# Performance work log

Measured on AMD Instinct MI355X. Metric: run time of the kernel, lower is better.

## Reference

```python
import jax, jax.numpy as jnp
import numpy as np

EMBED_DIM = 1024
HEAD_NUM = 16
HEAD_DIM = EMBED_DIM // HEAD_NUM
T, B, S = 2048, 4, 2048


def setup_inputs() -> dict:
    key = jax.random.key(0)
    ks = jax.random.split(key, 11)
    s = 0.02
    return {
        "query": jax.random.normal(ks[0], (T, B, EMBED_DIM), jnp.float32),
        "key": jax.random.normal(ks[1], (S, B, EMBED_DIM), jnp.float32),
        "value": jax.random.normal(ks[2], (S, B, EMBED_DIM), jnp.float32),
        "q_proj_weight": jax.random.normal(ks[3], (EMBED_DIM, EMBED_DIM), jnp.float32) * s,
        "k_proj_weight": jax.random.normal(ks[4], (EMBED_DIM, EMBED_DIM), jnp.float32) * s,
        "v_proj_weight": jax.random.normal(ks[5], (EMBED_DIM, EMBED_DIM), jnp.float32) * s,
        "in_proj_bias": jax.random.normal(ks[6], (3 * EMBED_DIM,), jnp.float32) * s,
        "bias_k": jax.random.normal(ks[7], (1, 1, EMBED_DIM), jnp.float32) * s,
        "bias_v": jax.random.normal(ks[8], (1, 1, EMBED_DIM), jnp.float32) * s,
        "out_proj_weight": jax.random.normal(ks[9], (EMBED_DIM, EMBED_DIM), jnp.float32) * s,
        "out_proj_bias": jax.random.normal(ks[10], (EMBED_DIM,), jnp.float32) * s,
    }


def reference(query, key, value, q_proj_weight, k_proj_weight, v_proj_weight,
              in_proj_bias, bias_k, bias_v, out_proj_weight, out_proj_bias):
    t, b, e = query.shape
    h, hd = HEAD_NUM, HEAD_DIM
    scaling = float(hd) ** -0.5
    # input projections (F.linear: x @ W.T + b)
    q = (query @ q_proj_weight.T + in_proj_bias[:e]) * scaling          # [T,B,E]
    k = key @ k_proj_weight.T + in_proj_bias[e:2 * e]                   # [S,B,E]
    v = value @ v_proj_weight.T + in_proj_bias[2 * e:]                  # [S,B,E]
    # append bias_k / bias_v token along the sequence dim
    k = jnp.concatenate([k, jnp.broadcast_to(bias_k, (1, b, e))], axis=0)  # [S+1,B,E]
    v = jnp.concatenate([v, jnp.broadcast_to(bias_v, (1, b, e))], axis=0)  # [S+1,B,E]
    # split heads: [L, B, E] -> [B*H, L, hd]
    q = q.reshape(t, b * h, hd).transpose(1, 0, 2)
    k = k.reshape(-1, b * h, hd).transpose(1, 0, 2)
    v = v.reshape(-1, b * h, hd).transpose(1, 0, 2)
    # full O(T*S) attention, as in the original bmm->softmax->bmm
    weights = jax.nn.softmax(jnp.einsum('nqd,nkd->nqk', q, k), axis=-1)  # [B*H,T,S+1]
    out = jnp.einsum('nqk,nkd->nqd', weights, v)                         # [B*H,T,hd]
    out = out.transpose(1, 0, 2).reshape(t, b, e)
    out = out @ out_proj_weight.T + out_proj_bias
    avg_weights = weights.sum(axis=1) / h                                # [B*H,S+1]
    return out, avg_weights
```

## Files before the change

kernel.cpp:

```cpp
#include <hip/hip_runtime.h>

#define T_DIM 2048
#define B_DIM 4
#define S_DIM 2048
#define E_DIM 1024
#define H_NUM 16
#define HD    64
#define NH    64
#define SP1   2049
#define SPAD  2112
#define NCHUNK 33
#define NTOKE ((size_t)T_DIM * B_DIM * E_DIM)

typedef short bf16x8 __attribute__((ext_vector_type(8)));
typedef short bf16x4 __attribute__((ext_vector_type(4)));
typedef float f32x4  __attribute__((ext_vector_type(4)));
typedef float f32x16 __attribute__((ext_vector_type(16)));
typedef unsigned int u32;

#define QSCALE 0.18033688011112042f

#if __has_builtin(__builtin_amdgcn_exp2f)
__device__ __forceinline__ float exp2_fast(float x) { return __builtin_amdgcn_exp2f(x); }
#else
__device__ __forceinline__ float exp2_fast(float x) { return __expf(x * 0.6931471805599453f); }
#endif

__device__ __forceinline__ unsigned short f2bf(float x) {
    union { float f; unsigned int u; } v; v.f = x;
    unsigned int r = v.u + 0x7FFFu + ((v.u >> 16) & 1u);
    return (unsigned short)(r >> 16);
}

__device__ __forceinline__ u32 cvtpk_bf16(float lo, float hi) {
    u32 r;
    asm("v_cvt_pk_bf16_f32 %0, %1, %2" : "=v"(r) : "v"(lo), "v"(hi));
    return r;
}
__device__ __forceinline__ void plswap(u32& a, u32& b) {
    asm("v_permlane32_swap_b32 %0, %1" : "+v"(a), "+v"(b));
}
__device__ __forceinline__ float max3f(float a, float b, float c) {
    float d;
    asm("v_max3_f32 %0, %1, %2, %3" : "=v"(d) : "v"(a), "v"(b), "v"(c));
    return d;
}

__device__ __forceinline__ void load_lds16(const void* g, void* l) {
    __builtin_amdgcn_global_load_lds(
        (const __attribute__((address_space(1))) unsigned int*)g,
        (__attribute__((address_space(3))) unsigned int*)l, 16, 0, 0);
}

__global__ __launch_bounds__(256)
void cvt_all(const float* __restrict__ q, const float* __restrict__ k,
             const float* __restrict__ v, const float* __restrict__ w0,
             const float* __restrict__ w1, const float* __restrict__ w2,
             const float* __restrict__ w3, short* __restrict__ indst,
             short* __restrict__ wdst, short* __restrict__ k_h,
             short* __restrict__ v_h, const float* __restrict__ bias_k,
             const float* __restrict__ bias_v)
{
    const int y = blockIdx.y;
    if (y < 3) {
        const float* src = (y == 0) ? q : (y == 1) ? k : v;
        short* d = indst + (size_t)y * NTOKE;
        const size_t i = (size_t)blockIdx.x * 256 + threadIdx.x;
        const float4* s = reinterpret_cast<const float4*>(src) + i * 2;
        float4 a = s[0], b = s[1];
        uint4 o;
        o.x = cvtpk_bf16(a.x, a.y); o.y = cvtpk_bf16(a.z, a.w);
        o.z = cvtpk_bf16(b.x, b.y); o.w = cvtpk_bf16(b.z, b.w);
        *(reinterpret_cast<uint4*>(d) + i) = o;
    } else {
        const size_t gi = (size_t)blockIdx.x * 256 + threadIdx.x;
        const size_t per = (size_t)E_DIM * E_DIM / 8;
        if (gi < 4 * per) {
            const int wsel = (int)(gi / per);
            const size_t i = gi % per;
            const float* src = (wsel == 0) ? w0 : (wsel == 1) ? w1 : (wsel == 2) ? w2 : w3;
            short* d = wdst + (size_t)wsel * E_DIM * E_DIM;
            const float4* s = reinterpret_cast<const float4*>(src) + i * 2;
            float4 a = s[0], b = s[1];
            uint4 o;
            o.x = cvtpk_bf16(a.x, a.y); o.y = cvtpk_bf16(a.z, a.w);
            o.z = cvtpk_bf16(b.x, b.y); o.w = cvtpk_bf16(b.z, b.w);
            *(reinterpret_cast<uint4*>(d) + i) = o;
        } else {
            const size_t fi = gi - 4 * per;
            if (fi < (size_t)(SPAD - S_DIM) * NH * HD) {
                const int d   = (int)(fi & 63);
                const int row = (int)((fi >> 6) & 63);
                const int n   = (int)(fi >> 12);
                short bk = 0, bv = 0;
                if (row == 0) {
                    bk = (short)f2bf(bias_k[(n & 15) * HD + d]);
                    bv = (short)f2bf(bias_v[(n & 15) * HD + d]);
                }
                const size_t idx = ((size_t)n * SPAD + S_DIM + row) * HD + d;
                k_h[idx] = bk;
                v_h[idx] = bv;
            }
        }
    }
}

__global__ __launch_bounds__(256, 4)
void gemm_qkv(const short* __restrict__ Abase, const short* __restrict__ Wall,
              const float* __restrict__ biasAll, short* __restrict__ outp)
{
    __shared__ short As[2][128][32];
    __shared__ short Bs[2][128][32];
    const int bm = blockIdx.x, bn = blockIdx.y;
    const int z = blockIdx.z;
    const short* Az = Abase + (size_t)z * NTOKE;
    const short* W  = Wall + (size_t)z * E_DIM * E_DIM;
    const float* bias = biasAll + z * E_DIM;

    const int tid = threadIdx.x;
    const int l = tid & 63, w = tid >> 6;
    const int wr = w >> 1, wc = w & 1;
    const int lr = l & 15, lg = l >> 4;
    const int srow = tid >> 2, scol = (tid & 3) * 8;

    auto stage = [&](int b, int k0) {
#pragma unroll
        for (int r = 0; r < 2; ++r) {
            const int row = r * 64 + srow;
            load_lds16(Az + (size_t)(bm * 128 + row) * E_DIM + k0 + scol, &As[b][row][scol]);
            load_lds16(W + (size_t)(bn * 128 + row) * E_DIM + k0 + scol, &Bs[b][row][scol]);
        }
    };

    stage(0, 0);
    __syncthreads();

    f32x4 acc[4][4] = {};
    int buf = 0;

    for (int k0 = 0; k0 < E_DIM; k0 += 32) {
        if (k0 + 32 < E_DIM) stage(buf ^ 1, k0 + 32);

        __builtin_amdgcn_s_setprio(1);
        bf16x8 af[4], bf[4];
#pragma unroll
        for (int mi = 0; mi < 4; ++mi)
            af[mi] = *reinterpret_cast<const bf16x8*>(&As[buf][wr * 64 + mi * 16 + lr][lg * 8]);
#pragma unroll
        for (int ni = 0; ni < 4; ++ni)
            bf[ni] = *reinterpret_cast<const bf16x8*>(&Bs[buf][wc * 64 + ni * 16 + lr][lg * 8]);
#pragma unroll
        for (int mi = 0; mi < 4; ++mi)
#pragma unroll
            for (int ni = 0; ni < 4; ++ni)
                acc[mi][ni] = __builtin_amdgcn_mfma_f32_16x16x32_bf16(
                    af[mi], bf[ni], acc[mi][ni], 0, 0, 0);
        __builtin_amdgcn_s_setprio(0);
        __syncthreads();
        buf ^= 1;
    }

#pragma unroll
    for (int mi = 0; mi < 4; ++mi)
#pragma unroll
        for (int ni = 0; ni < 4; ++ni) {
            const int colg = bn * 128 + wc * 64 + ni * 16 + lr;
            const float bv = bias[colg];
#pragma unroll
            for (int r = 0; r < 4; ++r) {
                const int m = bm * 128 + wr * 64 + mi * 16 + lg * 4 + r;
                float v = acc[mi][ni][r] + bv;
                if (z == 0) v *= QSCALE;
                const int seq = m >> 2, b = m & 3;
                const int head = colg >> 6, d = colg & 63;
                const int sd = (z == 0) ? T_DIM : SPAD;
                short* ob = outp;
                if (z == 1) ob += (size_t)NH * T_DIM * HD;
                else if (z == 2) ob += (size_t)NH * T_DIM * HD + (size_t)NH * SPAD * HD;
                ob[((size_t)(b * 16 + head) * sd + seq) * HD + d] = (short)f2bf(v);
            }
        }
}

__global__ __launch_bounds__(256, 2)
void gemm_out(const short* __restrict__ o_h, const short* __restrict__ wob,
              const float* __restrict__ out_b, float* __restrict__ out)
{
    __shared__ short As[2][128][64];
    __shared__ short Bs[2][128][64];
    const int bm = blockIdx.x, bn = blockIdx.y;

    const int tid = threadIdx.x;
    const int l = tid & 63, w = tid >> 6;
    const int wr = w >> 1, wc = w & 1;
    const int lr = l & 15, lg = l >> 4;
    const int srow = tid >> 3, scol = (tid & 7) * 8;

    auto stage = [&](int b, int k0) {
#pragma unroll
        for (int r = 0; r < 4; ++r) {
            const int row = r * 32 + srow;
            const int m = bm * 128 + row;
            const short* ga = o_h +
                ((size_t)((m & 3) * 16 + (k0 >> 6)) * T_DIM + (m >> 2)) * HD + scol;
            load_lds16(ga, &As[b][row][scol]);
            load_lds16(wob + (size_t)(bn * 128 + row) * E_DIM + k0 + scol, &Bs[b][row][scol]);
        }
    };

    stage(0, 0);
    __syncthreads();

    f32x4 acc[4][4] = {};
    int buf = 0;

    for (int k0 = 0; k0 < E_DIM; k0 += 64) {
        if (k0 + 64 < E_DIM) stage(buf ^ 1, k0 + 64);

        __builtin_amdgcn_s_setprio(1);
#pragma unroll
        for (int c = 0; c < 2; ++c) {
            bf16x8 af[4], bf[4];
#pragma unroll
            for (int mi = 0; mi < 4; ++mi)
                af[mi] = *reinterpret_cast<const bf16x8*>(&As[buf][wr * 64 + mi * 16 + lr][c * 32 + lg * 8]);
#pragma unroll
            for (int ni = 0; ni < 4; ++ni)
                bf[ni] = *reinterpret_cast<const bf16x8*>(&Bs[buf][wc * 64 + ni * 16 + lr][c * 32 + lg * 8]);
#pragma unroll
            for (int mi = 0; mi < 4; ++mi)
#pragma unroll
                for (int ni = 0; ni < 4; ++ni)
                    acc[mi][ni] = __builtin_amdgcn_mfma_f32_16x16x32_bf16(
                        af[mi], bf[ni], acc[mi][ni], 0, 0, 0);
        }
        __builtin_amdgcn_s_setprio(0);
        __syncthreads();
        buf ^= 1;
    }

#pragma unroll
    for (int mi = 0; mi < 4; ++mi)
#pragma unroll
        for (int ni = 0; ni < 4; ++ni) {
            const int colg = bn * 128 + wc * 64 + ni * 16 + lr;
            const float bv = out_b[colg];
#pragma unroll
            for (int r = 0; r < 4; ++r) {
                const int m = bm * 128 + wr * 64 + mi * 16 + lg * 4 + r;
                out[(size_t)m * E_DIM + colg] = acc[mi][ni][r] + bv;
            }
        }
}

__global__ __launch_bounds__(512, 4)
void attn_mfma(const short* __restrict__ q_h, const short* __restrict__ k_h,
               const short* __restrict__ v_h, short* __restrict__ o_h,
               float* __restrict__ m_arr, float* __restrict__ l_arr)
{
    __shared__ short KsD[2][64 * 64];
    __shared__ short VtD[2][64 * 64];

    const int id = blockIdx.x;
    const int xcd = id & 7, slot = id >> 3;
    const int n = xcd * 8 + (slot >> 3);
    const int q0 = (slot & 7) * 256;

    const int tid = threadIdx.x, l = tid & 63, w = tid >> 6;
    const int ql = l & 31;
    const int hi = l >> 5;
    const int qrow = q0 + w * 32 + ql;

    const int krow = tid >> 3, kcg = tid & 7;
    const int kswz = (kcg * 16) ^ ((krow & 7) << 4);
    const int sp = tid & 31, dq = tid >> 5;

    const short* kbase = k_h + (size_t)n * SPAD * HD;
    const short* vbase = v_h + (size_t)n * SPAD * HD;

    bf16x8 aq0, aq1, aq2, aq3;
    {
        const short* qp = q_h + ((size_t)n * T_DIM + qrow) * HD + hi * 8;
        aq0 = *(const bf16x8*)(qp);
        aq1 = *(const bf16x8*)(qp + 16);
        aq2 = *(const bf16x8*)(qp + 32);
        aq3 = *(const bf16x8*)(qp + 48);
    }

    bf16x8 pk  = *(const bf16x8*)(kbase + (size_t)krow * HD + kcg * 8);
    bf16x4 pva = *(const bf16x4*)(vbase + (size_t)(2 * sp) * HD + dq * 4);
    bf16x4 pvb = *(const bf16x4*)(vbase + (size_t)(2 * sp + 1) * HD + dq * 4);
    {
        char* KsB = (char*)KsD[0];
        char* VtB = (char*)VtD[0];
        *(bf16x8*)(KsB + krow * 128 + kswz) = pk;
#pragma unroll
        for (int j = 0; j < 4; ++j) {
            u32 pkd = (u32)(unsigned short)pva[j] | ((u32)(unsigned short)pvb[j] << 16);
            const int d = dq * 4 + j;
            *(u32*)(VtB + d * 128 + ((4 * sp) ^ ((d & 7) << 4))) = pkd;
        }
    }
    __syncthreads();

    float m_run = 0.0f;
    float l_run = 0.0f;
    f32x16 accA, accB;
#pragma unroll
    for (int r = 0; r < 16; ++r) { accA[r] = 0.f; accB[r] = 0.f; }

    for (int kc = 0; kc < NCHUNK; ++kc) {
        const char* KsB = (const char*)KsD[kc & 1];
        const char* VtB = (const char*)VtD[kc & 1];
        const bool more = (kc + 1 < NCHUNK);

        if (more) {
            const int s0n = (kc + 1) * 64;
            pk  = *(const bf16x8*)(kbase + (size_t)(s0n + krow) * HD + kcg * 8);
            pva = *(const bf16x4*)(vbase + (size_t)(s0n + 2 * sp) * HD + dq * 4);
            pvb = *(const bf16x4*)(vbase + (size_t)(s0n + 2 * sp + 1) * HD + dq * 4);
        }

        f32x16 sc0, sc1;
        const float nm = -m_run;
#pragma unroll
        for (int r = 0; r < 16; ++r) { sc0[r] = nm; sc1[r] = nm; }
        __builtin_amdgcn_s_setprio(1);
#pragma unroll
        for (int sl = 0; sl < 4; ++sl) {
            const int cb = ((sl * 32) + hi * 16) ^ ((ql & 7) << 4);
            bf16x8 kf0 = *(const bf16x8*)(KsB + ql * 128 + cb);
            bf16x8 kf1 = *(const bf16x8*)(KsB + (32 + ql) * 128 + cb);
            bf16x8 qf = (sl == 0) ? aq0 : (sl == 1) ? aq1 : (sl == 2) ? aq2 : aq3;
            sc0 = __builtin_amdgcn_mfma_f32_32x32x16_bf16(kf0, qf, sc0, 0, 0, 0);
            sc1 = __builtin_amdgcn_mfma_f32_32x32x16_bf16(kf1, qf, sc1, 0, 0, 0);
        }
        __builtin_amdgcn_s_setprio(0);

        const int s0 = kc * 64;
        if (s0 + 64 > SP1) {
#pragma unroll
            for (int r = 0; r < 16; ++r) {
                const int key = (r & 3) + 8 * (r >> 2) + 4 * hi;
                if (s0 + key >= SP1)      sc0[r] = -1e30f;
                if (s0 + 32 + key >= SP1) sc1[r] = -1e30f;
            }
        }

        float a0 = max3f(sc0[0],  sc0[1],  sc0[2]);
        float a1 = max3f(sc0[3],  sc0[4],  sc0[5]);
        float a2 = max3f(sc0[6],  sc0[7],  sc0[8]);
        float a3 = max3f(sc0[9],  sc0[10], sc0[11]);
        float a4 = max3f(sc0[12], sc0[13], sc0[14]);
        float a5 = max3f(sc0[15], sc1[0],  sc1[1]);
        float a6 = max3f(sc1[2],  sc1[3],  sc1[4]);
        float a7 = max3f(sc1[5],  sc1[6],  sc1[7]);
        float a8 = max3f(sc1[8],  sc1[9],  sc1[10]);
        float a9 = max3f(sc1[11], sc1[12], sc1[13]);
        float aA = fmaxf(sc1[14], sc1[15]);
        float b0 = max3f(a0, a1, a2);
        float b1 = max3f(a3, a4, a5);
        float b2 = max3f(a6, a7, a8);
        float b3 = fmaxf(a9, aA);
        float mxl = fmaxf(max3f(b0, b1, b2), b3);
        const float mx = fmaxf(mxl, __shfl_xor(mxl, 32));
        if (!__all(mx <= 8.0f)) {
            const float sh = fmaxf(mx, 0.0f);
            const float fac = exp2_fast(-sh);
            l_run *= fac;
#pragma unroll
            for (int r = 0; r < 16; ++r) {
                accA[r] *= fac; accB[r] *= fac;
                sc0[r] -= sh;   sc1[r] -= sh;
            }
            m_run += sh;
        }
        float p0[16], p1[16];
#pragma unroll
        for (int r = 0; r < 16; ++r) p0[r] = exp2_fast(sc0[r]);
#pragma unroll
        for (int r = 0; r < 16; ++r) p1[r] = exp2_fast(sc1[r]);
        float sv[16];
#pragma unroll
        for (int r = 0; r < 16; ++r) sv[r] = p0[r] + p1[r];
#pragma unroll
        for (int s = 8; s > 0; s >>= 1)
#pragma unroll
            for (int r = 0; r < s; ++r) sv[r] += sv[r + s];
        l_run += sv[0] + __shfl_xor(sv[0], 32);

        union PF { u32 u[4]; bf16x8 v; };
        PF pf0, pf1, pf2, pf3;
        {
            u32 a0_ = cvtpk_bf16(p0[0], p0[1]),   b0_ = cvtpk_bf16(p0[4], p0[5]);   plswap(a0_, b0_);
            u32 a1_ = cvtpk_bf16(p0[2], p0[3]),   b1_ = cvtpk_bf16(p0[6], p0[7]);   plswap(a1_, b1_);
            u32 a2_ = cvtpk_bf16(p0[8], p0[9]),   b2_ = cvtpk_bf16(p0[12], p0[13]); plswap(a2_, b2_);
            u32 a3_ = cvtpk_bf16(p0[10], p0[11]), b3_ = cvtpk_bf16(p0[14], p0[15]); plswap(a3_, b3_);
            pf0.u[0] = a0_; pf0.u[1] = a1_; pf0.u[2] = b0_; pf0.u[3] = b1_;
            pf1.u[0] = a2_; pf1.u[1] = a3_; pf1.u[2] = b2_; pf1.u[3] = b3_;
            u32 c0_ = cvtpk_bf16(p1[0], p1[1]),   d0_ = cvtpk_bf16(p1[4], p1[5]);   plswap(c0_, d0_);
            u32 c1_ = cvtpk_bf16(p1[2], p1[3]),   d1_ = cvtpk_bf16(p1[6], p1[7]);   plswap(c1_, d1_);
            u32 c2_ = cvtpk_bf16(p1[8], p1[9]),   d2_ = cvtpk_bf16(p1[12], p1[13]); plswap(c2_, d2_);
            u32 c3_ = cvtpk_bf16(p1[10], p1[11]), d3_ = cvtpk_bf16(p1[14], p1[15]); plswap(c3_, d3_);
            pf2.u[0] = c0_; pf2.u[1] = c1_; pf2.u[2] = d0_; pf2.u[3] = d1_;
            pf3.u[0] = c2_; pf3.u[1] = c3_; pf3.u[2] = d2_; pf3.u[3] = d3_;
        }

        __builtin_amdgcn_s_setprio(1);
#pragma unroll
        for (int ksl = 0; ksl < 4; ++ksl) {
            const int cb = ((ksl * 32) + hi * 16) ^ ((ql & 7) << 4);
            bf16x8 vf0 = *(const bf16x8*)(VtB + ql * 128 + cb);
            bf16x8 vf1 = *(const bf16x8*)(VtB + (32 + ql) * 128 + cb);
            const bf16x8 pv = (ksl == 0) ? pf0.v : (ksl == 1) ? pf1.v : (ksl == 2) ? pf2.v : pf3.v;
            accA = __builtin_amdgcn_mfma_f32_32x32x16_bf16(vf0, pv, accA, 0, 0, 0);
            accB = __builtin_amdgcn_mfma_f32_32x32x16_bf16(vf1, pv, accB, 0, 0, 0);
        }
        __builtin_amdgcn_s_setprio(0);

        if (more) {
            char* KsN = (char*)KsD[(kc & 1) ^ 1];
            char* VtN = (char*)VtD[(kc & 1) ^ 1];
            *(bf16x8*)(KsN + krow * 128 + kswz) = pk;
#pragma unroll
            for (int j = 0; j < 4; ++j) {
                u32 pkd = (u32)(unsigned short)pva[j] | ((u32)(unsigned short)pvb[j] << 16);
                const int d = dq * 4 + j;
                *(u32*)(VtN + d * 128 + ((4 * sp) ^ ((d & 7) << 4))) = pkd;
            }
            __syncthreads();
        }
    }

    const float il = 1.0f / l_run;
    short* orow = o_h + ((size_t)n * T_DIM + qrow) * HD;
#pragma unroll
    for (int rq = 0; rq < 4; ++rq) {
        uint2 st;
        st.x = cvtpk_bf16(accA[rq * 4 + 0] * il, accA[rq * 4 + 1] * il);
        st.y = cvtpk_bf16(accA[rq * 4 + 2] * il, accA[rq * 4 + 3] * il);
        *(uint2*)(orow + rq * 8 + hi * 4) = st;
        uint2 st2;
        st2.x = cvtpk_bf16(accB[rq * 4 + 0] * il, accB[rq * 4 + 1] * il);
        st2.y = cvtpk_bf16(accB[rq * 4 + 2] * il, accB[rq * 4 + 3] * il);
        *(uint2*)(orow + 32 + rq * 8 + hi * 4) = st2;
    }
    if (hi == 0) {
        m_arr[n * T_DIM + qrow] = m_run;
        l_arr[n * T_DIM + qrow] = l_run;
    }
}

__global__ __launch_bounds__(256)
void colsum_mfma(const short* __restrict__ q_h, const short* __restrict__ k_h,
                 const float* __restrict__ m_arr, const float* __restrict__ l_arr,
                 float* __restrict__ avg_out)
{
    __shared__ short Qs[2][64][72];
    __shared__ float msh[2][64];
    __shared__ float lih[2][64];

    const int id = blockIdx.x;
    const int xcd = id & 7, slot = id >> 3;
    const int n = xcd * 8 + slot / 33;
    const int s0 = (slot % 33) * 64;

    const int tid = threadIdx.x, l = tid & 63, w = tid >> 6;
    const int lr = l & 15, lg = l >> 4;
    const int qr = tid >> 3, qcg = tid & 7;

    const short* qbase = q_h + (size_t)n * T_DIM * HD;

    bf16x8 ak[2];
#pragma unroll
    for (int c = 0; c < 2; ++c)
        ak[c] = *reinterpret_cast<const bf16x8*>(
            k_h + ((size_t)n * SPAD + s0 + w * 16 + lr) * HD + c * 32 + lg * 8);

    bf16x8 qa = *(const bf16x8*)(qbase + (size_t)qr * HD + qcg * 8);
    bf16x8 qb = *(const bf16x8*)(qbase + (size_t)(32 + qr) * HD + qcg * 8);
    float mlv = 0.f;
    if (tid < 64) mlv = m_arr[n * T_DIM + tid];
    else if (tid < 128) mlv = l_arr[n * T_DIM + tid - 64];
    *(bf16x8*)&Qs[0][qr][qcg * 8] = qa;
    *(bf16x8*)&Qs[0][32 + qr][qcg * 8] = qb;
    if (tid < 64) msh[0][tid] = mlv;
    else if (tid < 128) lih[0][tid - 64] = 1.0f / mlv;
    __syncthreads();

    float csum[4] = {0.f, 0.f, 0.f, 0.f};

    for (int it = 0; it < T_DIM / 64; ++it) {
        const int buf = it & 1;
        const bool more = (it + 1 < T_DIM / 64);
        if (more) {
            const int qo = (it + 1) * 64;
            qa = *(const bf16x8*)(qbase + (size_t)(qo + qr) * HD + qcg * 8);
            qb = *(const bf16x8*)(qbase + (size_t)(qo + 32 + qr) * HD + qcg * 8);
            if (tid < 64) mlv = m_arr[n * T_DIM + qo + tid];
            else if (tid < 128) mlv = l_arr[n * T_DIM + qo + tid - 64];
        }
        __builtin_amdgcn_s_setprio(1);
#pragma unroll
        for (int qt = 0; qt < 4; ++qt) {
            bf16x8 bq0 = *reinterpret_cast<const bf16x8*>(&Qs[buf][qt * 16 + lr][lg * 8]);
            bf16x8 bq1 = *reinterpret_cast<const bf16x8*>(&Qs[buf][qt * 16 + lr][32 + lg * 8]);
            const float mq = msh[buf][qt * 16 + lr];
            const float lq = lih[buf][qt * 16 + lr];
            f32x4 z;
#pragma unroll
            for (int r = 0; r < 4; ++r) z[r] = -mq;
            z = __builtin_amdgcn_mfma_f32_16x16x32_bf16(ak[0], bq0, z, 0, 0, 0);
            z = __builtin_amdgcn_mfma_f32_16x16x32_bf16(ak[1], bq1, z, 0, 0, 0);
#pragma unroll
            for (int r = 0; r < 4; ++r)
                csum[r] += exp2_fast(z[r]) * lq;
        }
        __builtin_amdgcn_s_setprio(0);
        if (more) {
            *(bf16x8*)&Qs[buf ^ 1][qr][qcg * 8] = qa;
            *(bf16x8*)&Qs[buf ^ 1][32 + qr][qcg * 8] = qb;
            if (tid < 64) msh[buf ^ 1][tid] = mlv;
            else if (tid < 128) lih[buf ^ 1][tid - 64] = 1.0f / mlv;
            __syncthreads();
        }
    }

#pragma unroll
    for (int r = 0; r < 4; ++r) {
        float v = csum[r];
        v += __shfl_xor(v, 1, 16);
        v += __shfl_xor(v, 2, 16);
        v += __shfl_xor(v, 4, 16);
        v += __shfl_xor(v, 8, 16);
        if (lr == 0) {
            const int key = s0 + w * 16 + lg * 4 + r;
            if (key < SP1) avg_out[(size_t)n * SP1 + key] = v * 0.0625f;
        }
    }
}

extern "C" void kernel_launch(void* const* d_in, const int* in_sizes, int n_in,
                              void* d_out, int out_size, void* d_ws, size_t ws_size,
                              hipStream_t stream)
{
    const float* query   = (const float*)d_in[0];
    const float* key     = (const float*)d_in[1];
    const float* value   = (const float*)d_in[2];
    const float* wq      = (const float*)d_in[3];
    const float* wk      = (const float*)d_in[4];
    const float* wv      = (const float*)d_in[5];
    const float* in_bias = (const float*)d_in[6];
    const float* bias_k  = (const float*)d_in[7];
    const float* bias_v  = (const float*)d_in[8];
    const float* wo      = (const float*)d_in[9];
    const float* out_b   = (const float*)d_in[10];
    float* out = (float*)d_out;

    short* wqb    = (short*)d_ws;
    short* wob    = wqb + (size_t)3 * E_DIM * E_DIM;
    short* qkv_bf = wqb + (size_t)4 * E_DIM * E_DIM;
    short* q_h = qkv_bf + 3 * NTOKE;
    short* k_h = q_h + (size_t)NH * T_DIM * HD;
    short* v_h = k_h + (size_t)NH * SPAD * HD;
    short* o_h = v_h + (size_t)NH * SPAD * HD;
    float* m_arr = (float*)(o_h + (size_t)NH * T_DIM * HD);
    float* l_arr = m_arr + (size_t)NH * T_DIM;

    const dim3 blk(256);
    hipLaunchKernelGGL(cvt_all, dim3(4096, 4), blk, 0, stream,
                       query, key, value, wq, wk, wv, wo, qkv_bf, wqb,
                       k_h, v_h, bias_k, bias_v);

    hipLaunchKernelGGL(gemm_qkv, dim3(64, 8, 3), blk, 0, stream,
                       qkv_bf, wqb, in_bias, q_h);
    hipLaunchKernelGGL(attn_mfma, dim3(512), dim3(512), 0, stream,
                       q_h, k_h, v_h, o_h, m_arr, l_arr);
    hipLaunchKernelGGL(colsum_mfma, dim3(2112), blk, 0, stream,
                       q_h, k_h, m_arr, l_arr, out + (size_t)T_DIM * B_DIM * E_DIM);
    hipLaunchKernelGGL(gemm_out, dim3(64, 8), blk, 0, stream,
                       o_h, wob, out_b, out);
}
```

Measured before the change: 279.3 us.

## Fuse fp32-to-bf16 activation conversion into QKV projection GEMM loads

Removes the separate conversion pass over query/key/value; the QKV GEMM now loads fp32 activation tiles into registers, converts them to bf16 and writes them to shared memory after the MFMA block. Weight conversion and K/V padding stay in a smaller prep kernel. This avoids writing and re-reading a bf16 copy of all activations, at the cost of fetching twice the bytes for A tiles in every GEMM block and using extra registers for the register-staged loads.

Result: no change. 277.3 us (-0.7%).

```diff
diff --git a/kernel.cpp b/kernel.cpp
--- a/kernel.cpp
+++ b/kernel.cpp
@@ -53,19 +53,19 @@
 }
 
 __global__ __launch_bounds__(256)
-void cvt_all(const float* __restrict__ q, const float* __restrict__ k,
-             const float* __restrict__ v, const float* __restrict__ w0,
-             const float* __restrict__ w1, const float* __restrict__ w2,
-             const float* __restrict__ w3, short* __restrict__ indst,
-             short* __restrict__ wdst, short* __restrict__ k_h,
-             short* __restrict__ v_h, const float* __restrict__ bias_k,
-             const float* __restrict__ bias_v)
+void cvt_wpad(const float* __restrict__ w0, const float* __restrict__ w1,
+              const float* __restrict__ w2, const float* __restrict__ w3,
+              short* __restrict__ wdst, short* __restrict__ k_h,
+              short* __restrict__ v_h, const float* __restrict__ bias_k,
+              const float* __restrict__ bias_v)
 {
-    const int y = blockIdx.y;
-    if (y < 3) {
-        const float* src = (y == 0) ? q : (y == 1) ? k : v;
-        short* d = indst + (size_t)y * NTOKE;
-        const size_t i = (size_t)blockIdx.x * 256 + threadIdx.x;
+    const size_t gi = (size_t)blockIdx.x * 256 + threadIdx.x;
+    const size_t per = (size_t)E_DIM * E_DIM / 8;
+    if (gi < 4 * per) {
+        const int wsel = (int)(gi / per);
+        const size_t i = gi % per;
+        const float* src = (wsel == 0) ? w0 : (wsel == 1) ? w1 : (wsel == 2) ? w2 : w3;
+        short* d = wdst + (size_t)wsel * E_DIM * E_DIM;
         const float4* s = reinterpret_cast<const float4*>(src) + i * 2;
         float4 a = s[0], b = s[1];
         uint4 o;
@@ -73,47 +73,33 @@
         o.z = cvtpk_bf16(b.x, b.y); o.w = cvtpk_bf16(b.z, b.w);
         *(reinterpret_cast<uint4*>(d) + i) = o;
     } else {
-        const size_t gi = (size_t)blockIdx.x * 256 + threadIdx.x;
-        const size_t per = (size_t)E_DIM * E_DIM / 8;
-        if (gi < 4 * per) {
-            const int wsel = (int)(gi / per);
-            const size_t i = gi % per;
-            const float* src = (wsel == 0) ? w0 : (wsel == 1) ? w1 : (wsel == 2) ? w2 : w3;
-            short* d = wdst + (size_t)wsel * E_DIM * E_DIM;
-            const float4* s = reinterpret_cast<const float4*>(src) + i * 2;
-            float4 a = s[0], b = s[1];
-            uint4 o;
-            o.x = cvtpk_bf16(a.x, a.y); o.y = cvtpk_bf16(a.z, a.w);
-            o.z = cvtpk_bf16(b.x, b.y); o.w = cvtpk_bf16(b.z, b.w);
-            *(reinterpret_cast<uint4*>(d) + i) = o;
-        } else {
-            const size_t fi = gi - 4 * per;
-            if (fi < (size_t)(SPAD - S_DIM) * NH * HD) {
-                const int d   = (int)(fi & 63);
-                const int row = (int)((fi >> 6) & 63);
-                const int n   = (int)(fi >> 12);
-                short bk = 0, bv = 0;
-                if (row == 0) {
-                    bk = (short)f2bf(bias_k[(n & 15) * HD + d]);
-                    bv = (short)f2bf(bias_v[(n & 15) * HD + d]);
-                }
-                const size_t idx = ((size_t)n * SPAD + S_DIM + row) * HD + d;
-                k_h[idx] = bk;
-                v_h[idx] = bv;
+        const size_t fi = gi - 4 * per;
+        if (fi < (size_t)(SPAD - S_DIM) * NH * HD) {
+            const int d   = (int)(fi & 63);
+            const int row = (int)((fi >> 6) & 63);
+            const int n   = (int)(fi >> 12);
+            short bk = 0, bv = 0;
+            if (row == 0) {
+                bk = (short)f2bf(bias_k[(n & 15) * HD + d]);
+                bv = (short)f2bf(bias_v[(n & 15) * HD + d]);
             }
+            const size_t idx = ((size_t)n * SPAD + S_DIM + row) * HD + d;
+            k_h[idx] = bk;
+            v_h[idx] = bv;
         }
     }
 }
 
 __global__ __launch_bounds__(256, 4)
-void gemm_qkv(const short* __restrict__ Abase, const short* __restrict__ Wall,
+void gemm_qkv(const float* __restrict__ Aq, const float* __restrict__ Ak,
+              const float* __restrict__ Av, const short* __restrict__ Wall,
               const float* __restrict__ biasAll, short* __restrict__ outp)
 {
     __shared__ short As[2][128][32];
     __shared__ short Bs[2][128][32];
     const int bm = blockIdx.x, bn = blockIdx.y;
     const int z = blockIdx.z;
-    const short* Az = Abase + (size_t)z * NTOKE;
+    const float* Af = (z == 0) ? Aq : (z == 1) ? Ak : Av;
     const short* W  = Wall + (size_t)z * E_DIM * E_DIM;
     const float* bias = biasAll + z * E_DIM;
 
@@ -123,23 +109,48 @@
     const int lr = l & 15, lg = l >> 4;
     const int srow = tid >> 2, scol = (tid & 3) * 8;
 
-    auto stage = [&](int b, int k0) {
+    float4 fa0, fa1, fb0, fb1;
+
+    auto loadA = [&](int k0) {
+        const float* ap0 = Af + (size_t)(bm * 128 + srow) * E_DIM + k0 + scol;
+        fa0 = *reinterpret_cast<const float4*>(ap0);
+        fa1 = *reinterpret_cast<const float4*>(ap0 + 4);
+        const float* ap1 = ap0 + (size_t)64 * E_DIM;
+        fb0 = *reinterpret_cast<const float4*>(ap1);
+        fb1 = *reinterpret_cast<const float4*>(ap1 + 4);
+    };
+    auto writeA = [&](int b) {
+        uint4 wv;
+        wv.x = cvtpk_bf16(fa0.x, fa0.y); wv.y = cvtpk_bf16(fa0.z, fa0.w);
+        wv.z = cvtpk_bf16(fa1.x, fa1.y); wv.w = cvtpk_bf16(fa1.z, fa1.w);
+        *reinterpret_cast<uint4*>(&As[b][srow][scol]) = wv;
+        uint4 wv2;
+        wv2.x = cvtpk_bf16(fb0.x, fb0.y); wv2.y = cvtpk_bf16(fb0.z, fb0.w);
+        wv2.z = cvtpk_bf16(fb1.x, fb1.y); wv2.w = cvtpk_bf16(fb1.z, fb1.w);
+        *reinterpret_cast<uint4*>(&As[b][64 + srow][scol]) = wv2;
+    };
+    auto stageW = [&](int b, int k0) {
 #pragma unroll
         for (int r = 0; r < 2; ++r) {
             const int row = r * 64 + srow;
-            load_lds16(Az + (size_t)(bm * 128 + row) * E_DIM + k0 + scol, &As[b][row][scol]);
             load_lds16(W + (size_t)(bn * 128 + row) * E_DIM + k0 + scol, &Bs[b][row][scol]);
         }
     };
 
-    stage(0, 0);
+    loadA(0);
+    writeA(0);
+    stageW(0, 0);
     __syncthreads();
 
     f32x4 acc[4][4] = {};
     int buf = 0;
 
     for (int k0 = 0; k0 < E_DIM; k0 += 32) {
-        if (k0 + 32 < E_DIM) stage(buf ^ 1, k0 + 32);
+        const bool more = (k0 + 32 < E_DIM);
+        if (more) {
+            stageW(buf ^ 1, k0 + 32);
+            loadA(k0 + 32);
+        }
 
         __builtin_amdgcn_s_setprio(1);
         bf16x8 af[4], bf[4];
@@ -156,6 +167,8 @@
                 acc[mi][ni] = __builtin_amdgcn_mfma_f32_16x16x32_bf16(
                     af[mi], bf[ni], acc[mi][ni], 0, 0, 0);
         __builtin_amdgcn_s_setprio(0);
+
+        if (more) writeA(buf ^ 1);
         __syncthreads();
         buf ^= 1;
     }
@@ -557,10 +570,9 @@
     const float* out_b   = (const float*)d_in[10];
     float* out = (float*)d_out;
 
-    short* wqb    = (short*)d_ws;
-    short* wob    = wqb + (size_t)3 * E_DIM * E_DIM;
-    short* qkv_bf = wqb + (size_t)4 * E_DIM * E_DIM;
-    short* q_h = qkv_bf + 3 * NTOKE;
+    short* wqb = (short*)d_ws;
+    short* wob = wqb + (size_t)3 * E_DIM * E_DIM;
+    short* q_h = wqb + (size_t)4 * E_DIM * E_DIM;
     short* k_h = q_h + (size_t)NH * T_DIM * HD;
     short* v_h = k_h + (size_t)NH * SPAD * HD;
     short* o_h = v_h + (size_t)NH * SPAD * HD;
@@ -568,12 +580,11 @@
     float* l_arr = m_arr + (size_t)NH * T_DIM;
 
     const dim3 blk(256);
-    hipLaunchKernelGGL(cvt_all, dim3(4096, 4), blk, 0, stream,
-                       query, key, value, wq, wk, wv, wo, qkv_bf, wqb,
-                       k_h, v_h, bias_k, bias_v);
+    hipLaunchKernelGGL(cvt_wpad, dim3(3072), blk, 0, stream,
+                       wq, wk, wv, wo, wqb, k_h, v_h, bias_k, bias_v);
 
     hipLaunchKernelGGL(gemm_qkv, dim3(64, 8, 3), blk, 0, stream,
-                       qkv_bf, wqb, in_bias, q_h);
+                       query, key, value, wqb, in_bias, q_h);
     hipLaunchKernelGGL(attn_mfma, dim3(512), dim3(512), 0, stream,
                        q_h, k_h, v_h, o_h, m_arr, l_arr);
     hipLaunchKernelGGL(colsum_mfma, dim3(2112), blk, 0, stream,
```
